# Kernel tuning notes

Hardware: AMD Instinct MI355X
Metric: run time of the kernel (lower is better)

Reference implementation:

```python
import jax, jax.numpy as jnp
import numpy as np

D_MODEL = 512
D_STATE = 64
LN_EPS = 1e-3  # Keras LayerNormalization default epsilon


def setup_inputs() -> dict:
    key = jax.random.key(0)
    ks = jax.random.split(key, 12)
    B, S, D, N = 8, 4096, D_MODEL, D_STATE

    def glorot(k, shape):
        fan_in, fan_out = shape[0], shape[1]
        lim = np.sqrt(6.0 / (fan_in + fan_out)).astype(np.float32)
        return jax.random.uniform(k, shape, jnp.float32, -lim, lim)

    return {
        "x": jax.random.normal(ks[0], (B, S, D), jnp.float32),
        "ln_gamma": jnp.ones((D,), jnp.float32),
        "ln_beta": jnp.zeros((D,), jnp.float32),
        "W_in": glorot(ks[1], (D, D)),
        "b_in": jnp.zeros((D,), jnp.float32),
        "W_xs": glorot(ks[2], (D, N)),
        "W_B": glorot(ks[3], (D, N)),
        "b_B": jnp.zeros((N,), jnp.float32),
        "W_C": glorot(ks[4], (D, N)),
        "b_C": jnp.zeros((N,), jnp.float32),
        "A_log": jax.random.uniform(ks[5], (N,), jnp.float32, -4.0, -1.0),
        "D_skip": jnp.ones((D,), jnp.float32),
        "W_so": glorot(ks[6], (N, D)),
        "W_out": glorot(ks[7], (D, D)),
        "b_out": jnp.zeros((D,), jnp.float32),
    }


def reference(x, ln_gamma, ln_beta, W_in, b_in, W_xs, W_B, b_B, W_C, b_C,
              A_log, D_skip, W_so, W_out, b_out):
    residual = x
    # LayerNorm over last axis (Keras default eps=1e-3)
    mu = jnp.mean(x, axis=-1, keepdims=True)
    var = jnp.mean(jnp.square(x - mu), axis=-1, keepdims=True)
    xn = (x - mu) * jax.lax.rsqrt(var + LN_EPS) * ln_gamma + ln_beta
    # input projection (this projected x is what feeds the D skip too)
    xp = xn @ W_in + b_in                      # [B, S, D]
    Bmat = xp @ W_B + b_B                      # [B, S, N] selective B(x)
    Cmat = xp @ W_C + b_C                      # [B, S, N] selective C(x)
    xs = xp @ W_xs                             # [B, S, N]
    A_bar = jnp.exp(-jnp.exp(A_log))           # [N], stable decay in (0,1)
    Bx = Bmat * xs                             # per-step drive B_t * x_state_t

    # sequential scan: h_t = A_bar * h_{t-1} + Bx_t
    def step(h, bx):
        h = A_bar * h + bx
        return h, h

    h0 = jnp.zeros((x.shape[0], A_log.shape[0]), x.dtype)
    _, hs = jax.lax.scan(step, h0, jnp.swapaxes(Bx, 0, 1))  # hs: [S, B, N]
    hs = jnp.swapaxes(hs, 0, 1)                             # [B, S, N]

    y = jnp.einsum('bsn,nd->bsd', Cmat * hs, W_so) + D_skip * xp
    y = y @ W_out + b_out
    # dropout is identity at inference (training=None)
    return y + residual
```

## Files before the change

### kernel.cpp

```cpp
#include <hip/hip_runtime.h>
#include <cstdint>
#include <cstddef>


typedef unsigned short bf16_t;
typedef __attribute__((ext_vector_type(8))) short bh8;
typedef __attribute__((ext_vector_type(4))) float f4;

#define M_ROWS 32768
#define SCAN_L 32
#define SCAN_C 128

__device__ __forceinline__ unsigned short f2bf(float f) {
  union { float f; unsigned int u; } c; c.f = f;
  unsigned int u = c.u;
  return (unsigned short)((u + 0x7FFFu + ((u >> 16) & 1u)) >> 16);
}

__device__ __forceinline__ uint2 pack4bf(f4 a) {
  uint2 r;
  r.x = (unsigned)f2bf(a[0]) | ((unsigned)f2bf(a[1]) << 16);
  r.y = (unsigned)f2bf(a[2]) | ((unsigned)f2bf(a[3]) << 16);
  return r;
}

__device__ __forceinline__ void async_cp16(void* lds, const void* g) {
  __builtin_amdgcn_global_load_lds((const __attribute__((address_space(1))) void*)g,
                                   (__attribute__((address_space(3))) void*)lds, 16, 0, 0);
}

__global__ __launch_bounds__(256) void prep_all(
    const float* __restrict__ W_in, const float* __restrict__ W_out,
    const float* __restrict__ W_so, const float* __restrict__ W_xs,
    const float* __restrict__ W_B,  const float* __restrict__ W_C,
    const float* __restrict__ b_in, const float* __restrict__ D_skip,
    const float* __restrict__ A_log,
    bf16_t* __restrict__ Wout_t, bf16_t* __restrict__ Wdout_t,
    bf16_t* __restrict__ Win_b, bf16_t* __restrict__ Wso_b,
    bf16_t* __restrict__ Wcat_t, bf16_t* __restrict__ Wproj,
    float* __restrict__ Abar, float* __restrict__ Apow) {
  int i = blockIdx.x * 256 + threadIdx.x;
  if (i < 262144) { int k = i >> 9, n = i & 511;
    Wout_t[(size_t)n * 512 + k] = f2bf(W_out[k * 512 + n]); return; }
  i -= 262144;
  if (i < 262144) { int k = i >> 9, n = i & 511;
    Wdout_t[(size_t)n * 512 + k] = f2bf(D_skip[k] * W_out[k * 512 + n]); return; }
  i -= 262144;
  if (i < 262144) { Win_b[i] = f2bf(W_in[i]); return; }
  i -= 262144;
  if (i < 65536) { int r = i >> 9, j = i & 511;
    Win_b[(size_t)(512 + r) * 512 + j] = (r == 0) ? f2bf(b_in[j]) : (bf16_t)0; return; }
  i -= 65536;
  if (i < 65536) { int k = i >> 9, j = i & 511;
    Wso_b[i] = (k < 64) ? f2bf(W_so[k * 512 + j]) : (bf16_t)0; return; }
  i -= 65536;
  if (i < 131072) { int k = i >> 8, n = i & 255;
    float v = 0.f;
    if (n < 64)       v = W_xs[k * 64 + n];
    else if (n < 128) v = W_B[k * 64 + n - 64];
    else if (n < 192) v = W_C[k * 64 + n - 128];
    Wcat_t[(size_t)n * 512 + k] = f2bf(v); return; }
  i -= 131072;
  if (i < 32768) { int r = i >> 9, d = i & 511;
    Wproj[(size_t)(192 + r) * 512 + d] = 0; return; }
  i -= 32768;
  if (i < 64) {
    float a = __expf(A_log[i]);
    Abar[i] = __expf(-a);
    Apow[i] = __expf(-a * (float)SCAN_L);
  }
}

__global__ __launch_bounds__(256, 4) void gemm_prep(
    const bf16_t* __restrict__ Win_b, const bf16_t* __restrict__ Wcat_t,
    const bf16_t* __restrict__ Wso_b, const bf16_t* __restrict__ Wout_t,
    const bf16_t* __restrict__ Wdout_t,
    const float* __restrict__ b_B, const float* __restrict__ b_C,
    bf16_t* __restrict__ Wproj, bf16_t* __restrict__ Wcat2,
    float* __restrict__ biasp, float* __restrict__ biasW2) {
  __shared__ __align__(16) bf16_t As[128 * 64];
  __shared__ __align__(16) bf16_t Bs[128 * 64];
  const int tid = threadIdx.x;
  const int wave = tid >> 6, lane = tid & 63;
  const int quad = lane >> 4, l16 = lane & 15;
  const int wm = (wave >> 1) * 64, wn = (wave & 1) * 64;
  int role, mb, nb;
  if (blockIdx.x < 10)      { role = 0; mb = blockIdx.x >> 1; nb = blockIdx.x & 1; }
  else if (blockIdx.x < 14) { role = 1; mb = 0; nb = blockIdx.x - 10; }
  else { role = 2; int t = blockIdx.x - 14; mb = t >> 2; nb = t & 3; }
  const bf16_t* Ap = (role == 1) ? Wso_b : Win_b;
  const bf16_t* Bp = (role == 0) ? Wcat_t : (role == 1) ? Wout_t : Wdout_t;

  f4 acc[4][4];
  #pragma unroll
  for (int i = 0; i < 4; ++i)
    #pragma unroll
    for (int j = 0; j < 4; ++j) acc[i][j] = (f4){0.f, 0.f, 0.f, 0.f};

  for (int kt = 0; kt < 8; ++kt) {
    const int k0 = kt << 6;
    __syncthreads();
    #pragma unroll
    for (int i = 0; i < 4; ++i) {
      const int base = (wave * 4 + i) * 64;
      const int cid = base + lane;
      const int row = cid >> 3;
      const int g = (cid & 7) ^ (row & 7);
      async_cp16((char*)As + base * 16,
                 Ap + (size_t)(mb * 128 + row) * 512 + k0 + g * 8);
    }
    #pragma unroll
    for (int i = 0; i < 4; ++i) {
      const int base = (wave * 4 + i) * 64;
      const int cid = base + lane;
      const int row = cid >> 3;
      const int g = (cid & 7) ^ (row & 7);
      async_cp16((char*)Bs + base * 16,
                 Bp + (size_t)(nb * 128 + row) * 512 + k0 + g * 8);
    }
    __syncthreads();
    #pragma unroll
    for (int ks = 0; ks < 2; ++ks) {
      const int gb = ks * 4 + quad;
      bh8 af[4], bfv[4];
      #pragma unroll
      for (int im = 0; im < 4; ++im) {
        const int row = wm + im * 16 + l16;
        af[im] = *(const bh8*)((const char*)As + row * 128 + ((gb ^ (row & 7)) * 16));
      }
      #pragma unroll
      for (int in_ = 0; in_ < 4; ++in_) {
        const int row = wn + in_ * 16 + l16;
        bfv[in_] = *(const bh8*)((const char*)Bs + row * 128 + ((gb ^ (row & 7)) * 16));
      }
      #pragma unroll
      for (int im = 0; im < 4; ++im)
        #pragma unroll
        for (int in_ = 0; in_ < 4; ++in_)
          acc[im][in_] = __builtin_amdgcn_mfma_f32_16x16x32_bf16(af[im], bfv[in_],
                                                                 acc[im][in_], 0, 0, 0);
    }
  }

  #pragma unroll
  for (int im = 0; im < 4; ++im) {
    #pragma unroll
    for (int in_ = 0; in_ < 4; ++in_) {
      const int row0 = mb * 128 + wm + im * 16 + quad * 4;
      const int col = nb * 128 + wn + in_ * 16 + l16;
      if (role == 0) {
        if (col < 192) {
          if (row0 < 512) {
            *(uint2*)(Wproj + (size_t)col * 512 + row0) = pack4bf(acc[im][in_]);
          } else if (row0 == 512) {
            float v = acc[im][in_][0];
            if (col >= 128)     v += b_C[col - 128];
            else if (col >= 64) v += b_B[col - 64];
            biasp[col] = v;
          }
        }
      } else if (role == 1) {
        if (row0 < 64)
          *(uint2*)(Wcat2 + (size_t)col * 576 + row0) = pack4bf(acc[im][in_]);
      } else {
        if (row0 < 512) {
          *(uint2*)(Wcat2 + (size_t)col * 576 + 64 + row0) = pack4bf(acc[im][in_]);
        } else if (row0 == 512) {
          biasW2[col] = acc[im][in_][0];
        }
      }
    }
  }
}

__global__ __launch_bounds__(256) void ln_kernel(
    const float* __restrict__ x, const float* __restrict__ gamma,
    const float* __restrict__ beta, bf16_t* __restrict__ xn) {
  const int row = blockIdx.x * 4 + (threadIdx.x >> 6);
  const int lane = threadIdx.x & 63;
  const float* xr = x + (size_t)row * 512 + lane * 8;
  float4 v0 = *(const float4*)xr;
  float4 v1 = *(const float4*)(xr + 4);
  float s  = v0.x + v0.y + v0.z + v0.w + v1.x + v1.y + v1.z + v1.w;
  float sq = v0.x*v0.x + v0.y*v0.y + v0.z*v0.z + v0.w*v0.w
           + v1.x*v1.x + v1.y*v1.y + v1.z*v1.z + v1.w*v1.w;
  #pragma unroll
  for (int off = 32; off > 0; off >>= 1) {
    s  += __shfl_xor(s, off, 64);
    sq += __shfl_xor(sq, off, 64);
  }
  const float mu  = s * (1.0f / 512.0f);
  const float var = sq * (1.0f / 512.0f) - mu * mu;
  const float rs  = rsqrtf(var + 1e-3f);
  float4 g0 = *(const float4*)(gamma + lane * 8);
  float4 g1 = *(const float4*)(gamma + lane * 8 + 4);
  float4 b0 = *(const float4*)(beta + lane * 8);
  float4 b1 = *(const float4*)(beta + lane * 8 + 4);
  bh8 ov;
  ov[0] = (short)f2bf((v0.x - mu) * rs * g0.x + b0.x);
  ov[1] = (short)f2bf((v0.y - mu) * rs * g0.y + b0.y);
  ov[2] = (short)f2bf((v0.z - mu) * rs * g0.z + b0.z);
  ov[3] = (short)f2bf((v0.w - mu) * rs * g0.w + b0.w);
  ov[4] = (short)f2bf((v1.x - mu) * rs * g1.x + b1.x);
  ov[5] = (short)f2bf((v1.y - mu) * rs * g1.y + b1.y);
  ov[6] = (short)f2bf((v1.z - mu) * rs * g1.z + b1.z);
  ov[7] = (short)f2bf((v1.w - mu) * rs * g1.w + b1.w);
  *(bh8*)(xn + (size_t)row * 512 + lane * 8) = ov;
}

template <int MODE>
__global__ __launch_bounds__(256, 4) void gemm_mfma(
    const bf16_t* __restrict__ A0, const bf16_t* __restrict__ A1,
    const bf16_t* __restrict__ Wt, int K,
    float* __restrict__ outf,
    const float* __restrict__ bias0, const float* __restrict__ bias1,
    const float* __restrict__ resid) {
  __shared__ __align__(16) bf16_t As[128 * 64];
  __shared__ __align__(16) bf16_t Bs[128 * 64];
  const int tid = threadIdx.x;
  const int wave = tid >> 6, lane = tid & 63;
  const int quad = lane >> 4, l16 = lane & 15;
  const int wm = (wave >> 1) * 64, wn = (wave & 1) * 64;
  const int mb = blockIdx.x, nb = blockIdx.y;

  f4 acc[4][4];
  #pragma unroll
  for (int i = 0; i < 4; ++i)
    #pragma unroll
    for (int j = 0; j < 4; ++j) acc[i][j] = (f4){0.f, 0.f, 0.f, 0.f};

  const int nkt = K >> 6;
  for (int kt = 0; kt < nkt; ++kt) {
    const int k0 = kt << 6;
    const bf16_t* Ap; int lda, kk;
    if (MODE == 3) {
      if (kt == 0) { Ap = A0; lda = 64;  kk = 0; }
      else         { Ap = A1; lda = 512; kk = k0 - 64; }
    } else { Ap = A0; lda = K; kk = k0; }

    __syncthreads();
    #pragma unroll
    for (int i = 0; i < 4; ++i) {
      const int base = (wave * 4 + i) * 64;
      const int cid = base + lane;
      const int row = cid >> 3;
      const int g = (cid & 7) ^ (row & 7);
      async_cp16((char*)As + base * 16,
                 Ap + (size_t)(mb * 128 + row) * lda + kk + g * 8);
    }
    #pragma unroll
    for (int i = 0; i < 4; ++i) {
      const int base = (wave * 4 + i) * 64;
      const int cid = base + lane;
      const int row = cid >> 3;
      const int g = (cid & 7) ^ (row & 7);
      async_cp16((char*)Bs + base * 16,
                 Wt + (size_t)(nb * 128 + row) * K + k0 + g * 8);
    }
    __syncthreads();

    #pragma unroll
    for (int ks = 0; ks < 2; ++ks) {
      const int gb = ks * 4 + quad;
      bh8 af[4], bfv[4];
      #pragma unroll
      for (int im = 0; im < 4; ++im) {
        const int row = wm + im * 16 + l16;
        af[im] = *(const bh8*)((const char*)As + row * 128 + ((gb ^ (row & 7)) * 16));
      }
      #pragma unroll
      for (int in_ = 0; in_ < 4; ++in_) {
        const int row = wn + in_ * 16 + l16;
        bfv[in_] = *(const bh8*)((const char*)Bs + row * 128 + ((gb ^ (row & 7)) * 16));
      }
      #pragma unroll
      for (int im = 0; im < 4; ++im)
        #pragma unroll
        for (int in_ = 0; in_ < 4; ++in_)
          acc[im][in_] = __builtin_amdgcn_mfma_f32_16x16x32_bf16(af[im], bfv[in_],
                                                                 acc[im][in_], 0, 0, 0);
    }
  }

  #pragma unroll
  for (int im = 0; im < 4; ++im) {
    #pragma unroll
    for (int in_ = 0; in_ < 4; ++in_) {
      #pragma unroll
      for (int r = 0; r < 4; ++r) {
        const int row = mb * 128 + wm + im * 16 + quad * 4 + r;
        const int col = nb * 128 + wn + in_ * 16 + l16;
        float v = acc[im][in_][r];
        if (MODE == 2) {
          if (col < 192)
            outf[((size_t)(col >> 6) * M_ROWS + row) * 64 + (col & 63)] = v + bias1[col];
        } else {
          outf[(size_t)row * 512 + col] =
              v + bias0[col] + bias1[col] + resid[(size_t)row * 512 + col];
        }
      }
    }
  }
}

__global__ __launch_bounds__(64) void scan_chunk(
    const float* __restrict__ projP, const float* __restrict__ Abar,
    float* __restrict__ carryT) {
  const int b = blockIdx.x >> 7, c = blockIdx.x & (SCAN_C - 1), n = threadIdx.x;
  const float A = Abar[n];
  const size_t row0 = (size_t)b * 4096 + c * SCAN_L;
  const float* pxs = projP + row0 * 64;
  const float* pB  = projP + ((size_t)M_ROWS + row0) * 64;
  float h = 0.f;
  for (int i = 0; i < SCAN_L; ++i)
    h = fmaf(A, h, pxs[i * 64 + n] * pB[i * 64 + n]);
  carryT[((size_t)(b * 64 + n)) * SCAN_C + c] = h;
}

__global__ __launch_bounds__(64) void scan_apply(
    const float* __restrict__ projP, const float* __restrict__ Abar,
    const float* __restrict__ Apow, const float* __restrict__ carryT,
    bf16_t* __restrict__ CH) {
  const int b = blockIdx.x >> 7, c = blockIdx.x & (SCAN_C - 1), n = threadIdx.x;
  const float A = Abar[n];
  const float Ap = Apow[n];
  const float* cr = carryT + ((size_t)(b * 64 + n)) * SCAN_C;
  float h = 0.f;
  for (int j = 0; j < c; ++j) h = fmaf(Ap, h, cr[j]);
  const size_t row0 = (size_t)b * 4096 + c * SCAN_L;
  const float* pxs = projP + row0 * 64;
  const float* pB  = projP + ((size_t)M_ROWS + row0) * 64;
  const float* pC  = projP + ((size_t)2 * M_ROWS + row0) * 64;
  bf16_t* o = CH + row0 * 64;
  for (int i = 0; i < SCAN_L; ++i) {
    h = fmaf(A, h, pxs[i * 64 + n] * pB[i * 64 + n]);
    o[i * 64 + n] = f2bf(pC[i * 64 + n] * h);
  }
}

extern "C" void kernel_launch(void* const* d_in, const int* in_sizes, int n_in,
                              void* d_out, int out_size, void* d_ws, size_t ws_size,
                              hipStream_t stream) {
  const float* x      = (const float*)d_in[0];
  const float* ln_g   = (const float*)d_in[1];
  const float* ln_b   = (const float*)d_in[2];
  const float* W_in   = (const float*)d_in[3];
  const float* b_in   = (const float*)d_in[4];
  const float* W_xs   = (const float*)d_in[5];
  const float* W_B    = (const float*)d_in[6];
  const float* b_B    = (const float*)d_in[7];
  const float* W_C    = (const float*)d_in[8];
  const float* b_C    = (const float*)d_in[9];
  const float* A_log  = (const float*)d_in[10];
  const float* D_skip = (const float*)d_in[11];
  const float* W_so   = (const float*)d_in[12];
  const float* W_out  = (const float*)d_in[13];
  const float* b_out  = (const float*)d_in[14];
  float* out = (float*)d_out;

  char* w = (char*)d_ws;
  auto carve = [&](size_t bytes) {
    char* p = w; w += (bytes + 255) & ~(size_t)255; return p;
  };
  bf16_t* xn     = (bf16_t*)carve((size_t)M_ROWS * 512 * 2);
  float*  projP  = (float*)carve((size_t)3 * M_ROWS * 64 * 4);
  bf16_t* CH     = (bf16_t*)carve((size_t)M_ROWS * 64 * 2);
  float*  carryT = (float*)carve((size_t)8 * 64 * SCAN_C * 4);
  bf16_t* Wproj  = (bf16_t*)carve((size_t)256 * 512 * 2);
  bf16_t* Wcat2  = (bf16_t*)carve((size_t)512 * 576 * 2);
  bf16_t* Win_b  = (bf16_t*)carve((size_t)640 * 512 * 2);
  bf16_t* Wso_b  = (bf16_t*)carve((size_t)128 * 512 * 2);
  bf16_t* Wout_t = (bf16_t*)carve((size_t)512 * 512 * 2);
  bf16_t* Wdout_t= (bf16_t*)carve((size_t)512 * 512 * 2);
  bf16_t* Wcat_t = (bf16_t*)carve((size_t)256 * 512 * 2);
  float*  biasp  = (float*)carve(192 * 4);
  float*  biasW2 = (float*)carve(512 * 4);
  float*  Abar   = (float*)carve(256);
  float*  Apow   = (float*)carve(256);

  prep_all<<<4227, 256, 0, stream>>>(W_in, W_out, W_so, W_xs, W_B, W_C, b_in,
                                     D_skip, A_log, Wout_t, Wdout_t, Win_b,
                                     Wso_b, Wcat_t, Wproj, Abar, Apow);
  gemm_prep<<<34, 256, 0, stream>>>(Win_b, Wcat_t, Wso_b, Wout_t, Wdout_t,
                                    b_B, b_C, Wproj, Wcat2, biasp, biasW2);
  ln_kernel<<<8192, 256, 0, stream>>>(x, ln_g, ln_b, xn);
  gemm_mfma<2><<<dim3(256, 2), 256, 0, stream>>>(xn, nullptr, Wproj, 512,
                                                 projP, nullptr, biasp, nullptr);
  scan_chunk<<<8 * SCAN_C, 64, 0, stream>>>(projP, Abar, carryT);
  scan_apply<<<8 * SCAN_C, 64, 0, stream>>>(projP, Abar, Apow, carryT, CH);
  gemm_mfma<3><<<dim3(256, 4), 256, 0, stream>>>(CH, xn, Wcat2, 576,
                                                 out, b_out, biasW2, x);
}
```

Baseline: 238.2 us.

## Fuse Bx product into projection GEMM epilogue and stage stores through LDS

Reorders the concatenated projection weights so xs and B columns interleave in 16-wide groups, letting the projection GEMM epilogue multiply them and write only Bx and C, not three separate tensors. The scan kernels then read one precomputed Bx stream instead of two, which shrinks the projection buffer and scan traffic. The epilogues of both GEMM modes now stage accumulators through shared memory so global stores and residual loads are coalesced 16-byte vectors, and the output uses nontemporal stores. This adds a barrier and extra LDS traffic and depends on the interleaved column layout matching in the prep, bias and epilogue code.

```diff
diff --git a/kernel.cpp b/kernel.cpp
--- a/kernel.cpp
+++ b/kernel.cpp
@@ -56,9 +56,9 @@
   i -= 65536;
   if (i < 131072) { int k = i >> 8, n = i & 255;
     float v = 0.f;
-    if (n < 64)       v = W_xs[k * 64 + n];
-    else if (n < 128) v = W_B[k * 64 + n - 64];
-    else if (n < 192) v = W_C[k * 64 + n - 128];
+    if (n < 128) { int g = n >> 5, w = n & 31;
+      v = (w < 16) ? W_xs[k * 64 + g * 16 + w] : W_B[k * 64 + g * 16 + (w - 16)];
+    } else if (n < 192) v = W_C[k * 64 + n - 128];
     Wcat_t[(size_t)n * 512 + k] = f2bf(v); return; }
   i -= 131072;
   if (i < 32768) { int r = i >> 9, d = i & 511;
@@ -154,8 +154,9 @@
             *(uint2*)(Wproj + (size_t)col * 512 + row0) = pack4bf(acc[im][in_]);
           } else if (row0 == 512) {
             float v = acc[im][in_][0];
-            if (col >= 128)     v += b_C[col - 128];
-            else if (col >= 64) v += b_B[col - 64];
+            if (col < 128) { int w = col & 31;
+              if (w >= 16) v += b_B[(col >> 5) * 16 + (w - 16)];
+            } else v += b_C[col - 128];
             biasp[col] = v;
           }
         }
@@ -215,8 +216,9 @@
     float* __restrict__ outf,
     const float* __restrict__ bias0, const float* __restrict__ bias1,
     const float* __restrict__ resid) {
-  __shared__ __align__(16) bf16_t As[128 * 64];
-  __shared__ __align__(16) bf16_t Bs[128 * 64];
+  __shared__ __align__(16) char smem[32768];
+  bf16_t* As = (bf16_t*)smem;
+  bf16_t* Bs = (bf16_t*)(smem + 16384);
   const int tid = threadIdx.x;
   const int wave = tid >> 6, lane = tid & 63;
   const int quad = lane >> 4, l16 = lane & 15;
@@ -282,22 +284,72 @@
     }
   }
 
-  #pragma unroll
-  for (int im = 0; im < 4; ++im) {
-    #pragma unroll
-    for (int in_ = 0; in_ < 4; ++in_) {
-      #pragma unroll
-      for (int r = 0; r < 4; ++r) {
-        const int row = mb * 128 + wm + im * 16 + quad * 4 + r;
-        const int col = nb * 128 + wn + in_ * 16 + l16;
-        float v = acc[im][in_][r];
-        if (MODE == 2) {
-          if (col < 192)
-            outf[((size_t)(col >> 6) * M_ROWS + row) * 64 + (col & 63)] = v + bias1[col];
-        } else {
-          outf[(size_t)row * 512 + col] =
-              v + bias0[col] + bias1[col] + resid[(size_t)row * 512 + col];
-        }
+  __syncthreads();
+  float* lt = (float*)smem;
+
+  if (MODE == 2) {
+    if (nb == 0) {
+      float* wb = lt + wave * 2048;
+      #pragma unroll
+      for (int im = 0; im < 4; ++im)
+        #pragma unroll
+        for (int pp = 0; pp < 2; ++pp)
+          #pragma unroll
+          for (int r = 0; r < 4; ++r) {
+            const int c0 = wn + (2 * pp) * 16 + l16;
+            const float vx = acc[im][2 * pp][r]     + bias1[c0];
+            const float vb = acc[im][2 * pp + 1][r] + bias1[c0 + 16];
+            wb[(im * 16 + quad * 4 + r) * 32 + pp * 16 + l16] = vx * vb;
+          }
+      const int rsub = lane >> 3, cg8 = lane & 7;
+      #pragma unroll
+      for (int rr = 0; rr < 8; ++rr) {
+        const int rl = rr * 8 + rsub;
+        f4 v = *(f4*)(wb + rl * 32 + cg8 * 4);
+        const size_t row = (size_t)(mb * 128 + wm + rl);
+        *(f4*)(outf + row * 64 + (wn >> 1) + cg8 * 4) = v;
+      }
+    } else if (wn == 0) {
+      float* wb = lt + (wave >> 1) * 4096;
+      #pragma unroll
+      for (int im = 0; im < 4; ++im)
+        #pragma unroll
+        for (int in_ = 0; in_ < 4; ++in_)
+          #pragma unroll
+          for (int r = 0; r < 4; ++r) {
+            const int c = in_ * 16 + l16;
+            wb[(im * 16 + quad * 4 + r) * 64 + c] = acc[im][in_][r] + bias1[128 + c];
+          }
+      #pragma unroll
+      for (int rr = 0; rr < 16; ++rr) {
+        const int rl = rr * 4 + quad;
+        f4 v = *(f4*)(wb + rl * 64 + l16 * 4);
+        const size_t row = (size_t)(mb * 128 + wm + rl);
+        *(f4*)(outf + ((size_t)M_ROWS + row) * 64 + l16 * 4) = v;
+      }
+    }
+  } else {
+    const int gcol = nb * 128 + wn + l16 * 4;
+    f4 bsum = *(const f4*)(bias0 + gcol);
+    bsum += *(const f4*)(bias1 + gcol);
+    float* wb = lt + wave * 2048;
+    #pragma unroll
+    for (int p = 0; p < 2; ++p) {
+      #pragma unroll
+      for (int im2 = 0; im2 < 2; ++im2)
+        #pragma unroll
+        for (int in_ = 0; in_ < 4; ++in_)
+          #pragma unroll
+          for (int r = 0; r < 4; ++r)
+            wb[(im2 * 16 + quad * 4 + r) * 64 + in_ * 16 + l16] = acc[p * 2 + im2][in_][r];
+      #pragma unroll
+      for (int rr = 0; rr < 8; ++rr) {
+        const int rl = rr * 4 + quad;
+        f4 v = *(f4*)(wb + rl * 64 + l16 * 4);
+        const size_t row = (size_t)(mb * 128 + wm + p * 32 + rl);
+        f4 rv = *(const f4*)(resid + row * 512 + gcol);
+        f4 o = v + bsum + rv;
+        __builtin_nontemporal_store(o, (f4*)(outf + row * 512 + gcol));
       }
     }
   }
@@ -309,11 +361,10 @@
   const int b = blockIdx.x >> 7, c = blockIdx.x & (SCAN_C - 1), n = threadIdx.x;
   const float A = Abar[n];
   const size_t row0 = (size_t)b * 4096 + c * SCAN_L;
-  const float* pxs = projP + row0 * 64;
-  const float* pB  = projP + ((size_t)M_ROWS + row0) * 64;
+  const float* pBx = projP + row0 * 64;
   float h = 0.f;
   for (int i = 0; i < SCAN_L; ++i)
-    h = fmaf(A, h, pxs[i * 64 + n] * pB[i * 64 + n]);
+    h = fmaf(A, h, pBx[i * 64 + n]);
   carryT[((size_t)(b * 64 + n)) * SCAN_C + c] = h;
 }
 
@@ -328,12 +379,11 @@
   float h = 0.f;
   for (int j = 0; j < c; ++j) h = fmaf(Ap, h, cr[j]);
   const size_t row0 = (size_t)b * 4096 + c * SCAN_L;
-  const float* pxs = projP + row0 * 64;
-  const float* pB  = projP + ((size_t)M_ROWS + row0) * 64;
-  const float* pC  = projP + ((size_t)2 * M_ROWS + row0) * 64;
+  const float* pBx = projP + row0 * 64;
+  const float* pC  = projP + ((size_t)M_ROWS + row0) * 64;
   bf16_t* o = CH + row0 * 64;
   for (int i = 0; i < SCAN_L; ++i) {
-    h = fmaf(A, h, pxs[i * 64 + n] * pB[i * 64 + n]);
+    h = fmaf(A, h, pBx[i * 64 + n]);
     o[i * 64 + n] = f2bf(pC[i * 64 + n] * h);
   }
 }
@@ -363,7 +413,7 @@
     char* p = w; w += (bytes + 255) & ~(size_t)255; return p;
   };
   bf16_t* xn     = (bf16_t*)carve((size_t)M_ROWS * 512 * 2);
-  float*  projP  = (float*)carve((size_t)3 * M_ROWS * 64 * 4);
+  float*  projP  = (float*)carve((size_t)2 * M_ROWS * 64 * 4);
   bf16_t* CH     = (bf16_t*)carve((size_t)M_ROWS * 64 * 2);
   float*  carryT = (float*)carve((size_t)8 * 64 * SCAN_C * 4);
   bf16_t* Wproj  = (bf16_t*)carve((size_t)256 * 512 * 2);
```

After: 240.5 us. No clear change (+1.0%).
